# Kernel tuning notes

Hardware: AMD Instinct MI355X
Metric: run time of the kernel (lower is better)

The kernel has to match this reference:

```python
import jax, jax.numpy as jnp
import numpy as np


def _forward(agent_qs, ally_states, enemy_states, W_al, b_al, W_en, b_en, Wq, bq, Wk, bk,
             w1_W1, w1_b1, w1_W2, w1_b2, wf_W1, wf_b1, wf_W2, wf_b2, hb_W, hb_b,
             v_W1, v_b1, v_W2, v_b2):
    A, B, S, _ = ally_states.shape
    E = A + enemy_states.shape[0]
    D = W_al.shape[1]
    Da = Wq.shape[1]
    # entity encoders: [A,B,S,D], [En,B,S,D]
    ally_embed = ally_states @ W_al + b_al
    enemy_embed = enemy_states @ W_en + b_en
    entity = jnp.concatenate([ally_embed, enemy_embed], axis=0)      # [E,B,S,D]
    ent_bs = jnp.transpose(entity, (1, 2, 0, 3))                     # [B,S,E,D]
    q = ent_bs @ Wq + bq                                             # [B,S,E,Da]
    k = ent_bs @ Wk + bk                                             # [B,S,E,Da]
    scale = jnp.asarray(Da, q.dtype) ** 0.5
    energy = jnp.einsum('bsid,bsjd->bsij', q / scale, k)             # [B,S,E,E]
    # torch softmax(dim=1) on [BS,E,E] == softmax over the query axis i
    attn = jax.nn.softmax(energy, axis=2)
    # bmm(value[BS,D,E], attn).mean(-1) == value @ mean_j attn[:, :, e, j]
    attn_mean = jnp.mean(attn, axis=3)                               # [B,S,E]
    attn_out = jnp.einsum('bsed,bse->bsd', ent_bs, attn_mean)        # [B,S,D]
    ally_bs = jnp.transpose(ally_embed, (1, 2, 0, 3))                # [B,S,A,D]
    emi = jnp.concatenate(
        [jnp.broadcast_to(attn_out[:, :, None, :], (B, S, A, D)), ally_bs], axis=-1)  # [B,S,A,2D]
    # hypernets (2-layer)
    w1 = jnp.abs(jax.nn.relu(emi @ w1_W1 + w1_b1) @ w1_W2 + w1_b2)   # [B,S,A,M]
    b1 = attn_out @ hb_W + hb_b                                      # [B,S,M]
    hidden = jax.nn.elu(jnp.einsum('bsa,bsam->bsm', agent_qs, w1) + b1)
    wf = jnp.abs(jax.nn.relu(attn_out @ wf_W1 + wf_b1) @ wf_W2 + wf_b2)  # [B,S,M]
    v = jax.nn.relu(attn_out @ v_W1 + v_b1) @ v_W2 + v_b2            # [B,S,1]
    q_tot = jnp.einsum('bsm,bsm->bs', hidden, wf)[..., None] + v     # [B,S,1]
    return q_tot


def setup_inputs() -> dict:
    key = jax.random.key(0)
    B, S, A, En = 128, 128, 8, 8
    NFal, NFen, D, Da, M, H = 32, 16, 64, 128, 32, 64
    ks = jax.random.split(key, 32)
    p = lambda i, shape: jax.random.normal(ks[i], shape, dtype=jnp.float32) * 0.05
    return dict(
        agent_qs=jax.random.normal(ks[0], (B, S, A), dtype=jnp.float32),
        ally_states=jax.random.normal(ks[1], (A, B, S, NFal), dtype=jnp.float32),
        enemy_states=jax.random.normal(ks[2], (En, B, S, NFen), dtype=jnp.float32),
        W_al=p(3, (NFal, D)), b_al=p(4, (D,)), W_en=p(5, (NFen, D)), b_en=p(6, (D,)),
        Wq=p(7, (D, Da)), bq=p(8, (Da,)), Wk=p(9, (D, Da)), bk=p(10, (Da,)),
        w1_W1=p(11, (2 * D, H)), w1_b1=p(12, (H,)), w1_W2=p(13, (H, M)), w1_b2=p(14, (M,)),
        wf_W1=p(15, (D, H)), wf_b1=p(16, (H,)), wf_W2=p(17, (H, M)), wf_b2=p(18, (M,)),
        hb_W=p(19, (D, M)), hb_b=p(20, (M,)),
        v_W1=p(21, (D, M)), v_b1=p(22, (M,)), v_W2=p(23, (M, 1)), v_b2=p(24, (1,)),
    )


def reference(agent_qs, ally_states, enemy_states, W_al, b_al, W_en, b_en, Wq, bq, Wk, bk,
              w1_W1, w1_b1, w1_W2, w1_b2, wf_W1, wf_b1, wf_W2, wf_b2, hb_W, hb_b,
              v_W1, v_b1, v_W2, v_b2):
    return _forward(agent_qs, ally_states, enemy_states, W_al, b_al, W_en, b_en, Wq, bq, Wk, bk,
                    w1_W1, w1_b1, w1_W2, w1_b2, wf_W1, wf_b1, wf_W2, wf_b2, hb_W, hb_b,
                    v_W1, v_b1, v_W2, v_b2)
```

## Files before the change

kernel.cpp:

```cpp
#include <hip/hip_runtime.h>
#include <hip/hip_bf16.h>


#define B_   128
#define S_   128
#define BS_  (B_ * S_)
#define INV_S 0.08838834764831845f

typedef short bs8 __attribute__((ext_vector_type(8)));
typedef float f4  __attribute__((ext_vector_type(4)));

#define MFMA(a, b, c) __builtin_amdgcn_mfma_f32_16x16x32_bf16((a), (b), (c), 0, 0, 0)
#define LOADB(t) (*(const bs8*)&fb[(size_t)(t) * 512 + lane * 8])

__device__ __forceinline__ short f2bf(float f) {
    union { float f; unsigned u; } v; v.f = f;
    unsigned r = v.u + 0x7fffu + ((v.u >> 16) & 1u);
    return (short)(r >> 16);
}
__device__ __forceinline__ float bf2f(short s) {
    union { unsigned u; float f; } v;
    v.u = ((unsigned)(unsigned short)s) << 16;
    return v.f;
}

__global__ __launch_bounds__(64)
void qmix_pack(const float* __restrict__ Wq,   const float* __restrict__ Wk,
               const float* __restrict__ bk,
               const float* __restrict__ W_al, const float* __restrict__ W_en,
               const float* __restrict__ w1_W1, const float* __restrict__ w1_W2,
               const float* __restrict__ wf_W1, const float* __restrict__ hb_W,
               const float* __restrict__ v_W1,  const float* __restrict__ wf_W2,
               short* __restrict__ fb)
{
    const int blk = blockIdx.x, lane = threadIdx.x;
    const int quad = lane >> 4, l16 = lane & 15;
    bs8 v;
    if (blk < 8) {
        const int ks = blk >> 2, n = (blk & 3) * 16 + l16;
        float acc[8] = {0.f,0.f,0.f,0.f,0.f,0.f,0.f,0.f};
        const float4* wk4 = (const float4*)(Wk + n * 128);
        for (int t4 = 0; t4 < 32; ++t4) {
            const float4 wk = wk4[t4];
            #pragma unroll
            for (int j = 0; j < 8; ++j) {
                const float4 wq = *(const float4*)(Wq + (ks * 32 + quad * 8 + j) * 128 + t4 * 4);
                acc[j] += wq.x * wk.x + wq.y * wk.y + wq.z * wk.z + wq.w * wk.w;
            }
        }
        #pragma unroll
        for (int j = 0; j < 8; ++j) v[j] = f2bf(acc[j] * INV_S);
    } else if (blk < 16) {
        const bool en = (blk >= 12);
        const float* W = en ? W_en : W_al;
        const int Krows = en ? 16 : 32;
        const int n = ((blk - (en ? 12 : 8)) & 3) * 16 + l16;
        #pragma unroll
        for (int j = 0; j < 8; ++j) {
            const int k = quad * 8 + j;
            v[j] = (k < Krows) ? f2bf(W[k * 64 + n]) : (short)0;
        }
    } else if (blk < 32) {
        const int t = blk - 16, ks = t >> 2, n = (t & 3) * 16 + l16;
        #pragma unroll
        for (int j = 0; j < 8; ++j)
            v[j] = f2bf(w1_W1[(ks * 32 + quad * 8 + j) * 64 + n]);
    } else if (blk < 36) {
        const int t = blk - 32, ks = t >> 1, n = (t & 1) * 16 + l16;
        #pragma unroll
        for (int j = 0; j < 8; ++j)
            v[j] = f2bf(w1_W2[(ks * 32 + quad * 8 + j) * 32 + n]);
    } else if (blk < 38) {
        const int ks = blk - 36;
        float acc[8] = {0.f,0.f,0.f,0.f,0.f,0.f,0.f,0.f};
        const float4* bk4 = (const float4*)bk;
        for (int t4 = 0; t4 < 32; ++t4) {
            const float4 b = bk4[t4];
            #pragma unroll
            for (int j = 0; j < 8; ++j) {
                const float4 wq = *(const float4*)(Wq + (ks * 32 + quad * 8 + j) * 128 + t4 * 4);
                acc[j] += wq.x * b.x + wq.y * b.y + wq.z * b.z + wq.w * b.w;
            }
        }
        #pragma unroll
        for (int j = 0; j < 8; ++j)
            v[j] = (l16 == 0) ? f2bf(acc[j] * INV_S) : (short)0;
    } else if (blk < 54) {
        const int t = blk - 38, ks = t >> 3, n = (t & 7) * 16 + l16;
        #pragma unroll
        for (int j = 0; j < 8; ++j) {
            const int k = ks * 32 + quad * 8 + j;
            float w;
            if (n < 64)       w = wf_W1[k * 64 + n];
            else if (n < 96)  w = hb_W[k * 32 + (n - 64)];
            else              w = v_W1[k * 32 + (n - 96)];
            v[j] = f2bf(w);
        }
    } else {
        const int t = blk - 54, ks = t >> 1, n = (t & 1) * 16 + l16;
        #pragma unroll
        for (int j = 0; j < 8; ++j)
            v[j] = f2bf(wf_W2[(ks * 32 + quad * 8 + j) * 32 + n]);
    }
    *(bs8*)&fb[(size_t)blk * 512 + lane * 8] = v;
}

struct __align__(16) WaveLds {
    short ent[2][16][72];
    short scr[2][16][72];
    short aoutb[2][64];
    short hb16[2][64];
    float qs[2][8];
};

__global__ __launch_bounds__(128, 4)
void qmix_main(const float* __restrict__ agent_qs,
               const float* __restrict__ ally, const float* __restrict__ enemy,
               const float* __restrict__ b_al, const float* __restrict__ b_en,
               const float* __restrict__ w1_b1, const float* __restrict__ w1_b2,
               const float* __restrict__ wf_b1, const float* __restrict__ wf_b2,
               const float* __restrict__ hb_b,  const float* __restrict__ v_b1,
               const float* __restrict__ v_W2,  const float* __restrict__ v_b2,
               const short* __restrict__ fb,
               float* __restrict__ out)
{
    const int w    = threadIdx.x >> 6;
    const int lane = threadIdx.x & 63;
    const int quad = lane >> 4, l16 = lane & 15;
    const int half = lane >> 5;
    const int qh   = quad & 1;
    const int siteA = blockIdx.x * 4 + w * 2;

    __shared__ WaveLds lds[2];
    WaveLds& L = lds[w];

    if (lane < 16)
        L.qs[lane >> 3][lane & 7] =
            agent_qs[(size_t)(siteA + (lane >> 3)) * 8 + (lane & 7)];

    #pragma unroll
    for (int s = 0; s < 2; ++s) {
        const int site = siteA + s;
        bs8 a_al = {0,0,0,0,0,0,0,0}, a_en = {0,0,0,0,0,0,0,0};
        if (l16 < 8) {
            const float* pa = ally + ((size_t)l16 * BS_ + site) * 32 + quad * 8;
            const float4 f0 = *(const float4*)pa, f1 = *(const float4*)(pa + 4);
            a_al[0]=f2bf(f0.x); a_al[1]=f2bf(f0.y); a_al[2]=f2bf(f0.z); a_al[3]=f2bf(f0.w);
            a_al[4]=f2bf(f1.x); a_al[5]=f2bf(f1.y); a_al[6]=f2bf(f1.z); a_al[7]=f2bf(f1.w);
        } else if (quad < 2) {
            const float* pe = enemy + ((size_t)(l16 - 8) * BS_ + site) * 16 + quad * 8;
            const float4 f0 = *(const float4*)pe, f1 = *(const float4*)(pe + 4);
            a_en[0]=f2bf(f0.x); a_en[1]=f2bf(f0.y); a_en[2]=f2bf(f0.z); a_en[3]=f2bf(f0.w);
            a_en[4]=f2bf(f1.x); a_en[5]=f2bf(f1.y); a_en[6]=f2bf(f1.z); a_en[7]=f2bf(f1.w);
        }
        #pragma unroll
        for (int n0t = 0; n0t < 4; ++n0t) {
            f4 acc = {0.f, 0.f, 0.f, 0.f};
            acc = MFMA(a_al, LOADB(8 + n0t), acc);
            acc = MFMA(a_en, LOADB(12 + n0t), acc);
            const int d = n0t * 16 + l16;
            const float bal = b_al[d], ben = b_en[d];
            #pragma unroll
            for (int r = 0; r < 4; ++r) {
                const int row = quad * 4 + r;
                L.ent[s][row][d] = f2bf(acc[r] + (row < 8 ? bal : ben));
            }
        }
    }
    __syncthreads();

    bs8 ae0s[2], ae1s[2];
    #pragma unroll
    for (int s = 0; s < 2; ++s) {
        ae0s[s] = *(const bs8*)&L.ent[s][l16][quad * 8];
        ae1s[s] = *(const bs8*)&L.ent[s][l16][32 + quad * 8];
    }

    f4 pqs[2];
    #pragma unroll
    for (int s = 0; s < 2; ++s) {
        f4 pq = {0.f, 0.f, 0.f, 0.f};
        pq = MFMA(ae0s[s], LOADB(36), pq);
        pq = MFMA(ae1s[s], LOADB(37), pq);
        pqs[s] = pq;
        #pragma unroll
        for (int n0t = 0; n0t < 4; ++n0t) {
            f4 acc = {0.f, 0.f, 0.f, 0.f};
            acc = MFMA(ae0s[s], LOADB(0 + n0t), acc);
            acc = MFMA(ae1s[s], LOADB(4 + n0t), acc);
            const int d = n0t * 16 + l16;
            #pragma unroll
            for (int r = 0; r < 4; ++r) L.scr[s][quad * 4 + r][d] = f2bf(acc[r]);
        }
    }
    __syncthreads();

    #pragma unroll
    for (int s = 0; s < 2; ++s) {
        f4 eacc = {0.f, 0.f, 0.f, 0.f};
        {
            const bs8 at0 = *(const bs8*)&L.scr[s][l16][quad * 8];
            const bs8 at1 = *(const bs8*)&L.scr[s][l16][32 + quad * 8];
            eacc = MFMA(at0, ae0s[s], eacc);
            eacc = MFMA(at1, ae1s[s], eacc);
            const int src = lane & 48;
            #pragma unroll
            for (int r = 0; r < 4; ++r) eacc[r] += __shfl(pqs[s][r], src, 64);
        }
        float cmax = fmaxf(fmaxf(eacc[0], eacc[1]), fmaxf(eacc[2], eacc[3]));
        cmax = fmaxf(cmax, __shfl_xor(cmax, 16, 64));
        cmax = fmaxf(cmax, __shfl_xor(cmax, 32, 64));
        float er[4], csum = 0.f;
        #pragma unroll
        for (int r = 0; r < 4; ++r) { er[r] = __expf(eacc[r] - cmax); csum += er[r]; }
        csum += __shfl_xor(csum, 16, 64);
        csum += __shfl_xor(csum, 32, 64);
        const float inv = 1.f / csum;
        float amean[4];
        #pragma unroll
        for (int r = 0; r < 4; ++r) {
            float p = er[r] * inv;
            p += __shfl_xor(p, 1, 64);
            p += __shfl_xor(p, 2, 64);
            p += __shfl_xor(p, 4, 64);
            p += __shfl_xor(p, 8, 64);
            amean[r] = p * (1.f / 16.f);
        }
        #pragma unroll
        for (int n0t = 0; n0t < 4; ++n0t) {
            const int d = n0t * 16 + l16;
            float ap = amean[0] * bf2f(L.ent[s][quad * 4 + 0][d])
                     + amean[1] * bf2f(L.ent[s][quad * 4 + 1][d])
                     + amean[2] * bf2f(L.ent[s][quad * 4 + 2][d])
                     + amean[3] * bf2f(L.ent[s][quad * 4 + 3][d]);
            ap += __shfl_xor(ap, 16, 64);
            ap += __shfl_xor(ap, 32, 64);
            if (quad == 0) L.aoutb[s][d] = f2bf(ap);
        }
    }
    __syncthreads();

    const short* aoP = L.aoutb[l16 >> 3];
    const bs8 aab0 = *(const bs8*)&aoP[quad * 8];
    const bs8 aab1 = *(const bs8*)&aoP[32 + quad * 8];

    float xm[8];
    #pragma unroll
    for (int n0t = 0; n0t < 8; ++n0t) {
        f4 acc = {0.f, 0.f, 0.f, 0.f};
        acc = MFMA(aab0, LOADB(38 + n0t), acc);
        acc = MFMA(aab1, LOADB(46 + n0t), acc);
        xm[n0t] = acc[0];
    }
    #pragma unroll
    for (int n0t = 0; n0t < 4; ++n0t) {
        const int t = n0t * 16 + l16;
        L.hb16[half][t] = f2bf(fmaxf(xm[n0t] + wf_b1[t], 0.f));
    }
    const int m32 = lane & 31;
    const float b1m = xm[4 + qh] + hb_b[m32];
    float vsum;
    {
        float hv = fmaxf(xm[6 + qh] + v_b1[m32], 0.f) * v_W2[m32];
        hv += __shfl_xor(hv, 1, 64);
        hv += __shfl_xor(hv, 2, 64);
        hv += __shfl_xor(hv, 4, 64);
        hv += __shfl_xor(hv, 8, 64);
        hv += __shfl_xor(hv, 16, 64);
        vsum = hv;
    }
    __syncthreads();

    float wfm;
    {
        const short* hfP = L.hb16[l16 >> 3];
        const bs8 hf0 = *(const bs8*)&hfP[quad * 8];
        const bs8 hf1 = *(const bs8*)&hfP[32 + quad * 8];
        f4 acc0 = {0.f, 0.f, 0.f, 0.f};
        acc0 = MFMA(hf0, LOADB(54), acc0);
        acc0 = MFMA(hf1, LOADB(56), acc0);
        f4 acc1 = {0.f, 0.f, 0.f, 0.f};
        acc1 = MFMA(hf0, LOADB(55), acc1);
        acc1 = MFMA(hf1, LOADB(57), acc1);
        wfm = fabsf((qh ? acc1[0] : acc0[0]) + wf_b2[m32]);
    }

    {
        const short (*entP)[72] = (l16 < 8) ? L.ent[0] : L.ent[1];
        const bs8 ag0 = *(const bs8*)&entP[l16 & 7][quad * 8];
        const bs8 ag1 = *(const bs8*)&entP[l16 & 7][32 + quad * 8];
        #pragma unroll
        for (int n0t = 0; n0t < 4; ++n0t) {
            f4 acc = {0.f, 0.f, 0.f, 0.f};
            acc = MFMA(aab0, LOADB(16 + 0 + n0t), acc);
            acc = MFMA(aab1, LOADB(16 + 4 + n0t), acc);
            acc = MFMA(ag0,  LOADB(16 + 8 + n0t), acc);
            acc = MFMA(ag1,  LOADB(16 + 12 + n0t), acc);
            const int d = n0t * 16 + l16;
            const float b1v = w1_b1[d];
            #pragma unroll
            for (int r = 0; r < 4; ++r)
                L.scr[0][quad * 4 + r][d] = f2bf(fmaxf(acc[r] + b1v, 0.f));
        }
    }
    __syncthreads();

    float pm;
    {
        const bs8 ha0 = *(const bs8*)&L.scr[0][l16][quad * 8];
        const bs8 ha1 = *(const bs8*)&L.scr[0][l16][32 + quad * 8];
        const float* qsv = L.qs[half];
        float p0 = 0.f, p1 = 0.f;
        #pragma unroll
        for (int n0t = 0; n0t < 2; ++n0t) {
            f4 acc = {0.f, 0.f, 0.f, 0.f};
            acc = MFMA(ha0, LOADB(32 + 0 + n0t), acc);
            acc = MFMA(ha1, LOADB(32 + 2 + n0t), acc);
            const float b2v = w1_b2[n0t * 16 + l16];
            float p = 0.f;
            #pragma unroll
            for (int r = 0; r < 4; ++r)
                p += qsv[qh * 4 + r] * fabsf(acc[r] + b2v);
            if (n0t == 0) p0 = p; else p1 = p;
        }
        p0 += __shfl_xor(p0, 16, 64);
        p1 += __shfl_xor(p1, 16, 64);
        pm = qh ? p1 : p0;
    }

    float hp = pm + b1m;
    hp = (hp > 0.f) ? hp : (__expf(hp) - 1.f);
    float contrib = hp * wfm;
    contrib += __shfl_xor(contrib, 1, 64);
    contrib += __shfl_xor(contrib, 2, 64);
    contrib += __shfl_xor(contrib, 4, 64);
    contrib += __shfl_xor(contrib, 8, 64);
    contrib += __shfl_xor(contrib, 16, 64);
    if ((lane & 31) == 0)
        out[siteA + half] = contrib + vsum + v_b2[0];
}

extern "C" void kernel_launch(void* const* d_in, const int* in_sizes, int n_in,
                              void* d_out, int out_size, void* d_ws, size_t ws_size,
                              hipStream_t stream) {
    const float* p[25];
    for (int i = 0; i < 25; ++i) p[i] = (const float*)d_in[i];
    short* fb = (short*)d_ws;

    qmix_pack<<<58, 64, 0, stream>>>(p[7], p[9], p[10], p[3], p[5],
                                     p[11], p[13], p[15], p[19], p[21], p[17], fb);
    qmix_main<<<BS_ / 4, 128, 0, stream>>>(
        p[0], p[1], p[2], p[4], p[6], p[12], p[14],
        p[16], p[18], p[20], p[22], p[23], p[24],
        fb, (float*)d_out);
}
```

Baseline: 153.2 us.

## Replace block barriers with wave fences and keep encodings in registers

Each wave works only on its own LDS slice, so the block-wide __syncthreads calls are replaced with compiler-only memory fences. The entity embeddings are kept packed in registers rather than re-read from LDS. Several MFMAs are transposed so their results go to LDS as bs4 vector stores, agent_qs is loaded directly from global memory, and the value-head reduction is folded into the final shuffle reduction. The max-subtraction in the softmax is also dropped, which trades numerical safety against overflow for fewer shuffles; that only holds while the attention energies stay small.

```diff
diff --git a/kernel.cpp b/kernel.cpp
--- a/kernel.cpp
+++ b/kernel.cpp
@@ -8,20 +8,26 @@
 #define INV_S 0.08838834764831845f
 
 typedef short bs8 __attribute__((ext_vector_type(8)));
+typedef short bs4 __attribute__((ext_vector_type(4)));
 typedef float f4  __attribute__((ext_vector_type(4)));
 
 #define MFMA(a, b, c) __builtin_amdgcn_mfma_f32_16x16x32_bf16((a), (b), (c), 0, 0, 0)
 #define LOADB(t) (*(const bs8*)&fb[(size_t)(t) * 512 + lane * 8])
+#define FENCE() asm volatile("" ::: "memory")
 
 __device__ __forceinline__ short f2bf(float f) {
     union { float f; unsigned u; } v; v.f = f;
     unsigned r = v.u + 0x7fffu + ((v.u >> 16) & 1u);
     return (short)(r >> 16);
 }
-__device__ __forceinline__ float bf2f(short s) {
-    union { unsigned u; float f; } v;
-    v.u = ((unsigned)(unsigned short)s) << 16;
-    return v.f;
+__device__ __forceinline__ unsigned f2bf2(float lo, float hi) {
+    return (unsigned)(unsigned short)f2bf(lo) | ((unsigned)(unsigned short)f2bf(hi) << 16);
+}
+__device__ __forceinline__ float bf2f_lo(unsigned u) {
+    union { unsigned u; float f; } v; v.u = u << 16; return v.f;
+}
+__device__ __forceinline__ float bf2f_hi(unsigned u) {
+    union { unsigned u; float f; } v; v.u = u & 0xffff0000u; return v.f;
 }
 
 __global__ __launch_bounds__(64)
@@ -110,7 +116,6 @@
     short scr[2][16][72];
     short aoutb[2][64];
     short hb16[2][64];
-    float qs[2][8];
 };
 
 __global__ __launch_bounds__(128, 4)
@@ -134,9 +139,7 @@
     __shared__ WaveLds lds[2];
     WaveLds& L = lds[w];
 
-    if (lane < 16)
-        L.qs[lane >> 3][lane & 7] =
-            agent_qs[(size_t)(siteA + (lane >> 3)) * 8 + (lane & 7)];
+    unsigned encb[2][4][2];
 
     #pragma unroll
     for (int s = 0; s < 2; ++s) {
@@ -160,14 +163,18 @@
             acc = MFMA(a_en, LOADB(12 + n0t), acc);
             const int d = n0t * 16 + l16;
             const float bal = b_al[d], ben = b_en[d];
+            float vv[4];
             #pragma unroll
             for (int r = 0; r < 4; ++r) {
                 const int row = quad * 4 + r;
-                L.ent[s][row][d] = f2bf(acc[r] + (row < 8 ? bal : ben));
+                vv[r] = acc[r] + (row < 8 ? bal : ben);
+                L.ent[s][row][d] = f2bf(vv[r]);
             }
-        }
-    }
-    __syncthreads();
+            encb[s][n0t][0] = f2bf2(vv[0], vv[1]);
+            encb[s][n0t][1] = f2bf2(vv[2], vv[3]);
+        }
+    }
+    FENCE();
 
     bs8 ae0s[2], ae1s[2];
     #pragma unroll
@@ -184,16 +191,17 @@
         pq = MFMA(ae1s[s], LOADB(37), pq);
         pqs[s] = pq;
         #pragma unroll
-        for (int n0t = 0; n0t < 4; ++n0t) {
+        for (int mdt = 0; mdt < 4; ++mdt) {
             f4 acc = {0.f, 0.f, 0.f, 0.f};
-            acc = MFMA(ae0s[s], LOADB(0 + n0t), acc);
-            acc = MFMA(ae1s[s], LOADB(4 + n0t), acc);
-            const int d = n0t * 16 + l16;
-            #pragma unroll
-            for (int r = 0; r < 4; ++r) L.scr[s][quad * 4 + r][d] = f2bf(acc[r]);
-        }
-    }
-    __syncthreads();
+            acc = MFMA(LOADB(0 + mdt), ae0s[s], acc);
+            acc = MFMA(LOADB(4 + mdt), ae1s[s], acc);
+            bs4 tv;
+            #pragma unroll
+            for (int r = 0; r < 4; ++r) tv[r] = f2bf(acc[r]);
+            *(bs4*)&L.scr[s][l16][mdt * 16 + quad * 4] = tv;
+        }
+    }
+    FENCE();
 
     #pragma unroll
     for (int s = 0; s < 2; ++s) {
@@ -207,12 +215,9 @@
             #pragma unroll
             for (int r = 0; r < 4; ++r) eacc[r] += __shfl(pqs[s][r], src, 64);
         }
-        float cmax = fmaxf(fmaxf(eacc[0], eacc[1]), fmaxf(eacc[2], eacc[3]));
-        cmax = fmaxf(cmax, __shfl_xor(cmax, 16, 64));
-        cmax = fmaxf(cmax, __shfl_xor(cmax, 32, 64));
         float er[4], csum = 0.f;
         #pragma unroll
-        for (int r = 0; r < 4; ++r) { er[r] = __expf(eacc[r] - cmax); csum += er[r]; }
+        for (int r = 0; r < 4; ++r) { er[r] = __expf(eacc[r]); csum += er[r]; }
         csum += __shfl_xor(csum, 16, 64);
         csum += __shfl_xor(csum, 32, 64);
         const float inv = 1.f / csum;
@@ -226,23 +231,27 @@
             p += __shfl_xor(p, 8, 64);
             amean[r] = p * (1.f / 16.f);
         }
+        float sel = 0.f;
         #pragma unroll
         for (int n0t = 0; n0t < 4; ++n0t) {
-            const int d = n0t * 16 + l16;
-            float ap = amean[0] * bf2f(L.ent[s][quad * 4 + 0][d])
-                     + amean[1] * bf2f(L.ent[s][quad * 4 + 1][d])
-                     + amean[2] * bf2f(L.ent[s][quad * 4 + 2][d])
-                     + amean[3] * bf2f(L.ent[s][quad * 4 + 3][d]);
+            float ap = amean[0] * bf2f_lo(encb[s][n0t][0])
+                     + amean[1] * bf2f_hi(encb[s][n0t][0])
+                     + amean[2] * bf2f_lo(encb[s][n0t][1])
+                     + amean[3] * bf2f_hi(encb[s][n0t][1]);
             ap += __shfl_xor(ap, 16, 64);
             ap += __shfl_xor(ap, 32, 64);
-            if (quad == 0) L.aoutb[s][d] = f2bf(ap);
-        }
-    }
-    __syncthreads();
+            sel = (n0t == quad) ? ap : sel;
+        }
+        L.aoutb[s][quad * 16 + l16] = f2bf(sel);
+    }
+    FENCE();
 
     const short* aoP = L.aoutb[l16 >> 3];
     const bs8 aab0 = *(const bs8*)&aoP[quad * 8];
     const bs8 aab1 = *(const bs8*)&aoP[32 + quad * 8];
+    const short (*entP)[72] = (l16 < 8) ? L.ent[0] : L.ent[1];
+    const bs8 ag0 = *(const bs8*)&entP[l16 & 7][quad * 8];
+    const bs8 ag1 = *(const bs8*)&entP[l16 & 7][32 + quad * 8];
 
     float xm[8];
     #pragma unroll
@@ -253,23 +262,15 @@
         xm[n0t] = acc[0];
     }
     #pragma unroll
-    for (int n0t = 0; n0t < 4; ++n0t) {
-        const int t = n0t * 16 + l16;
-        L.hb16[half][t] = f2bf(fmaxf(xm[n0t] + wf_b1[t], 0.f));
+    for (int k = 0; k < 2; ++k) {
+        const int n0t = qh * 2 + k;
+        const int c = n0t * 16 + l16;
+        L.hb16[half][c] = f2bf(fmaxf(xm[n0t] + wf_b1[c], 0.f));
     }
     const int m32 = lane & 31;
     const float b1m = xm[4 + qh] + hb_b[m32];
-    float vsum;
-    {
-        float hv = fmaxf(xm[6 + qh] + v_b1[m32], 0.f) * v_W2[m32];
-        hv += __shfl_xor(hv, 1, 64);
-        hv += __shfl_xor(hv, 2, 64);
-        hv += __shfl_xor(hv, 4, 64);
-        hv += __shfl_xor(hv, 8, 64);
-        hv += __shfl_xor(hv, 16, 64);
-        vsum = hv;
-    }
-    __syncthreads();
+    const float hv = fmaxf(xm[6 + qh] + v_b1[m32], 0.f) * v_W2[m32];
+    FENCE();
 
     float wfm;
     {
@@ -285,42 +286,37 @@
         wfm = fabsf((qh ? acc1[0] : acc0[0]) + wf_b2[m32]);
     }
 
-    {
-        const short (*entP)[72] = (l16 < 8) ? L.ent[0] : L.ent[1];
-        const bs8 ag0 = *(const bs8*)&entP[l16 & 7][quad * 8];
-        const bs8 ag1 = *(const bs8*)&entP[l16 & 7][32 + quad * 8];
-        #pragma unroll
-        for (int n0t = 0; n0t < 4; ++n0t) {
-            f4 acc = {0.f, 0.f, 0.f, 0.f};
-            acc = MFMA(aab0, LOADB(16 + 0 + n0t), acc);
-            acc = MFMA(aab1, LOADB(16 + 4 + n0t), acc);
-            acc = MFMA(ag0,  LOADB(16 + 8 + n0t), acc);
-            acc = MFMA(ag1,  LOADB(16 + 12 + n0t), acc);
-            const int d = n0t * 16 + l16;
-            const float b1v = w1_b1[d];
-            #pragma unroll
-            for (int r = 0; r < 4; ++r)
-                L.scr[0][quad * 4 + r][d] = f2bf(fmaxf(acc[r] + b1v, 0.f));
-        }
-    }
-    __syncthreads();
+    #pragma unroll
+    for (int mt = 0; mt < 4; ++mt) {
+        f4 acc = {0.f, 0.f, 0.f, 0.f};
+        acc = MFMA(LOADB(16 + mt),      aab0, acc);
+        acc = MFMA(LOADB(16 + 4 + mt),  aab1, acc);
+        acc = MFMA(LOADB(16 + 8 + mt),  ag0,  acc);
+        acc = MFMA(LOADB(16 + 12 + mt), ag1,  acc);
+        const float4 b1v4 = *(const float4*)&w1_b1[mt * 16 + quad * 4];
+        bs4 hw;
+        hw[0] = f2bf(fmaxf(acc[0] + b1v4.x, 0.f));
+        hw[1] = f2bf(fmaxf(acc[1] + b1v4.y, 0.f));
+        hw[2] = f2bf(fmaxf(acc[2] + b1v4.z, 0.f));
+        hw[3] = f2bf(fmaxf(acc[3] + b1v4.w, 0.f));
+        *(bs4*)&L.scr[0][l16][mt * 16 + quad * 4] = hw;
+    }
+    FENCE();
 
     float pm;
     {
         const bs8 ha0 = *(const bs8*)&L.scr[0][l16][quad * 8];
         const bs8 ha1 = *(const bs8*)&L.scr[0][l16][32 + quad * 8];
-        const float* qsv = L.qs[half];
+        const float4 qsv4 = *(const float4*)&agent_qs[(size_t)(siteA + half) * 8 + qh * 4];
         float p0 = 0.f, p1 = 0.f;
         #pragma unroll
         for (int n0t = 0; n0t < 2; ++n0t) {
             f4 acc = {0.f, 0.f, 0.f, 0.f};
-            acc = MFMA(ha0, LOADB(32 + 0 + n0t), acc);
-            acc = MFMA(ha1, LOADB(32 + 2 + n0t), acc);
+            acc = MFMA(ha0, LOADB(32 + n0t), acc);
+            acc = MFMA(ha1, LOADB(34 + n0t), acc);
             const float b2v = w1_b2[n0t * 16 + l16];
-            float p = 0.f;
-            #pragma unroll
-            for (int r = 0; r < 4; ++r)
-                p += qsv[qh * 4 + r] * fabsf(acc[r] + b2v);
+            float p = qsv4.x * fabsf(acc[0] + b2v) + qsv4.y * fabsf(acc[1] + b2v)
+                    + qsv4.z * fabsf(acc[2] + b2v) + qsv4.w * fabsf(acc[3] + b2v);
             if (n0t == 0) p0 = p; else p1 = p;
         }
         p0 += __shfl_xor(p0, 16, 64);
@@ -330,14 +326,14 @@
 
     float hp = pm + b1m;
     hp = (hp > 0.f) ? hp : (__expf(hp) - 1.f);
-    float contrib = hp * wfm;
+    float contrib = hp * wfm + hv;
     contrib += __shfl_xor(contrib, 1, 64);
     contrib += __shfl_xor(contrib, 2, 64);
     contrib += __shfl_xor(contrib, 4, 64);
     contrib += __shfl_xor(contrib, 8, 64);
     contrib += __shfl_xor(contrib, 16, 64);
     if ((lane & 31) == 0)
-        out[siteA + half] = contrib + vsum + v_b2[0];
+        out[siteA + half] = contrib + v_b2[0];
 }
 
 extern "C" void kernel_launch(void* const* d_in, const int* in_sizes, int n_in,
```

Result: faster. 148.7 us (-3.0%).
